# Kernel optimization log

Measured on AMD Instinct MI355X. Metric: run time of the kernel, lower is better.

The kernel has to match this reference:

```python
import jax, jax.numpy as jnp
import numpy as np

D_MODEL = 1024
N_HEADS = 16
D_HEAD = D_MODEL // N_HEADS
HIDDEN = 4096
B, T = 2, 2048
EPS = 1e-5


def setup_inputs() -> dict:
    key = jax.random.key(0)
    ks = jax.random.split(key, 16)
    s = 0.02
    return {
        "x": jax.random.normal(ks[0], (B, T, D_MODEL), dtype=jnp.float32),
        # LayerNorm 1
        "gamma1": jnp.ones((D_MODEL,), jnp.float32),
        "beta1": jnp.zeros((D_MODEL,), jnp.float32),
        # attention projections, stored (in, out) so y = x @ W + b
        "Wq": jax.random.normal(ks[1], (D_MODEL, D_MODEL), jnp.float32) * s,
        "bq": jnp.zeros((D_MODEL,), jnp.float32),
        "Wk": jax.random.normal(ks[2], (D_MODEL, D_MODEL), jnp.float32) * s,
        "bk": jnp.zeros((D_MODEL,), jnp.float32),
        "Wv": jax.random.normal(ks[3], (D_MODEL, D_MODEL), jnp.float32) * s,
        "bv": jnp.zeros((D_MODEL,), jnp.float32),
        "Wo": jax.random.normal(ks[4], (D_MODEL, D_MODEL), jnp.float32) * s,
        "bo": jnp.zeros((D_MODEL,), jnp.float32),
        # LayerNorm 2
        "gamma2": jnp.ones((D_MODEL,), jnp.float32),
        "beta2": jnp.zeros((D_MODEL,), jnp.float32),
        # MLP
        "W1": jax.random.normal(ks[5], (D_MODEL, HIDDEN), jnp.float32) * s,
        "b1": jnp.zeros((HIDDEN,), jnp.float32),
        "W2": jax.random.normal(ks[6], (HIDDEN, D_MODEL), jnp.float32) * s,
        "b2": jnp.zeros((D_MODEL,), jnp.float32),
    }


def _layernorm(x, gamma, beta):
    mean = jnp.mean(x, axis=-1, keepdims=True)
    var = jnp.mean(jnp.square(x - mean), axis=-1, keepdims=True)  # unbiased=False
    return gamma * (x - mean) * jax.lax.rsqrt(var + EPS) + beta


def _attention(x, Wq, bq, Wk, bk, Wv, bv, Wo, bo):
    b, t, _ = x.shape
    q = (x @ Wq + bq).reshape(b, t, N_HEADS, D_HEAD)
    k = (x @ Wk + bk).reshape(b, t, N_HEADS, D_HEAD)
    v = (x @ Wv + bv).reshape(b, t, N_HEADS, D_HEAD)
    scores = jnp.einsum("bqhd,bkhd->bhqk", q, k) / np.sqrt(D_HEAD).astype(np.float32)
    causal = jnp.tril(jnp.ones((t, t), dtype=bool))  # keep j <= i
    scores = jnp.where(causal, scores, -jnp.inf)
    attn = jax.nn.softmax(scores, axis=-1)
    out = jnp.einsum("bhqk,bkhd->bqhd", attn, v).reshape(b, t, D_MODEL)
    return out @ Wo + bo


def reference(x, gamma1, beta1, Wq, bq, Wk, bk, Wv, bv, Wo, bo,
              gamma2, beta2, W1, b1, W2, b2):
    # x = x + Attn(LN1(x))
    x = x + _attention(_layernorm(x, gamma1, beta1), Wq, bq, Wk, bk, Wv, bv, Wo, bo)
    # x = x + MLP(LN2(x)); torch F.gelu default = exact erf gelu
    h = _layernorm(x, gamma2, beta2)
    h = jax.nn.gelu(h @ W1 + b1, approximate=False) @ W2 + b2
    return x + h
```

## Files before the change

### kernel.cpp

```cpp
#include <hip/hip_runtime.h>
#include <stdint.h>

typedef unsigned short u16;
typedef short bf16x8 __attribute__((ext_vector_type(8)));
typedef float f32x4 __attribute__((ext_vector_type(4)));
typedef float f32x16 __attribute__((ext_vector_type(16)));

#define MB (1024L*1024L)

__device__ inline u16 f2bf(float f) {
  union { float f; unsigned u; } v; v.f = f;
  unsigned r = (v.u + 0x7FFFu + ((v.u >> 16) & 1u)) >> 16;
  return (u16)r;
}

__device__ inline float bf2f(u16 u) {
  union { unsigned u; float f; } v; v.u = ((unsigned)u) << 16; return v.f;
}

__device__ inline unsigned cvtpk(float lo, float hi) {
  unsigned r;
  asm("v_cvt_pk_bf16_f32 %0, %1, %2" : "=v"(r) : "v"(lo), "v"(hi));
  return r;
}

#define GLOAD16(gptr, lptr) \
  __builtin_amdgcn_global_load_lds((__attribute__((address_space(1))) void*)(gptr), \
                                   (__attribute__((address_space(3))) void*)(lptr), 16, 0, 0)

__global__ __launch_bounds__(256) void twconv(const float* __restrict__ W,
                                              u16* __restrict__ WT, int K, int N) {
  __shared__ float tile[32][33];
  const int nbn = N >> 5;
  const int bk = blockIdx.x / nbn;
  const int bn = blockIdx.x % nbn;
  const int tid = threadIdx.x;
  const int r = tid >> 3;
  const int c4 = (tid & 7) << 2;
  const float4 v = *(const float4*)(W + (size_t)(bk * 32 + r) * N + bn * 32 + c4);
  tile[r][c4 + 0] = v.x; tile[r][c4 + 1] = v.y;
  tile[r][c4 + 2] = v.z; tile[r][c4 + 3] = v.w;
  __syncthreads();
  ushort4 o;
  o.x = f2bf(tile[c4 + 0][r]); o.y = f2bf(tile[c4 + 1][r]);
  o.z = f2bf(tile[c4 + 2][r]); o.w = f2bf(tile[c4 + 3][r]);
  *(ushort4*)(WT + (size_t)(bn * 32 + r) * K + bk * 32 + c4) = o;
}

__global__ __launch_bounds__(256) void concat3(const float* __restrict__ a,
                                               const float* __restrict__ b,
                                               const float* __restrict__ c,
                                               float* __restrict__ out, int n) {
  int i = blockIdx.x * 256 + threadIdx.x;
  if (i < n) { out[i] = a[i]; out[n + i] = b[i]; out[2 * n + i] = c[i]; }
}

__global__ __launch_bounds__(256) void ln_kernel(const float* __restrict__ x,
                                                 const float* __restrict__ gamma,
                                                 const float* __restrict__ beta,
                                                 u16* __restrict__ out) {
  const int row = blockIdx.x;
  const int tid = threadIdx.x;
  const float4 v = *(const float4*)(x + (size_t)row * 1024 + tid * 4);
  float s = v.x + v.y + v.z + v.w;
  float s2 = v.x * v.x + v.y * v.y + v.z * v.z + v.w * v.w;
#pragma unroll
  for (int m = 1; m < 64; m <<= 1) {
    s += __shfl_xor(s, m, 64);
    s2 += __shfl_xor(s2, m, 64);
  }
  __shared__ float red[8];
  const int w = tid >> 6;
  if ((tid & 63) == 0) { red[w] = s; red[4 + w] = s2; }
  __syncthreads();
  s = red[0] + red[1] + red[2] + red[3];
  s2 = red[4] + red[5] + red[6] + red[7];
  const float mean = s * (1.0f / 1024.0f);
  const float var = s2 * (1.0f / 1024.0f) - mean * mean;
  const float rstd = rsqrtf(var + 1e-5f);
  const float4 g = *(const float4*)(gamma + tid * 4);
  const float4 b = *(const float4*)(beta + tid * 4);
  ushort4 o;
  o.x = f2bf(g.x * (v.x - mean) * rstd + b.x);
  o.y = f2bf(g.y * (v.y - mean) * rstd + b.y);
  o.z = f2bf(g.z * (v.z - mean) * rstd + b.z);
  o.w = f2bf(g.w * (v.w - mean) * rstd + b.w);
  *(ushort4*)(out + (size_t)row * 1024 + tid * 4) = o;
}

template <int EPI, int BN>
__global__ __launch_bounds__(256, (BN == 64) ? 3 : 2)
void gemm_bt(const u16* __restrict__ A, const u16* __restrict__ BT,
             const float* __restrict__ bias, const float* __restrict__ res,
             void* __restrict__ outp, int M, int N, int K) {
  constexpr int MF = (BN == 128) ? 4 : 2;
  constexpr int ACH = 4;
  constexpr int BCH = BN / 32;
  constexpr int LOADS = ACH + BCH;
  __shared__ __align__(16) u16 As[2][128 * 64];
  __shared__ __align__(16) u16 Bs[2][BN * 64];
  const int nBN = N / BN;
  const int hw = blockIdx.x;
  const int xcd = hw & 7;
  const int rr = hw >> 3;
  const int bm = xcd * 4 + rr / nBN;
  const int bn = rr % nBN;
  const int tid = threadIdx.x;
  const int lane = tid & 63;
  const int wid = tid >> 6;
  const int wm = (BN == 128) ? (wid >> 1) : wid;
  const int wn = (BN == 128) ? (wid & 1) : 0;
  const int e4 = lane >> 4;

  int abase[MF], ax[MF];
#pragma unroll
  for (int m = 0; m < MF; ++m) {
    int rowa = wm * (MF * 16) + m * 16 + (lane & 15);
    abase[m] = rowa * 64; ax[m] = rowa & 7;
  }
  int bbase[4], bx[4];
#pragma unroll
  for (int n = 0; n < 4; ++n) {
    int rowb = wn * 64 + n * 16 + (lane & 15);
    bbase[n] = rowb * 64; bx[n] = rowb & 7;
  }

  size_t ga[ACH]; int loa[ACH];
#pragma unroll
  for (int c = 0; c < ACH; ++c) {
    int idx = tid + (c << 8);
    int row = idx >> 3;
    int ch = (idx & 7) ^ (row & 7);
    ga[c] = (size_t)(bm * 128 + row) * K + (ch << 3);
    loa[c] = idx << 4;
  }
  size_t gb[BCH]; int lob[BCH];
#pragma unroll
  for (int c = 0; c < BCH; ++c) {
    int idx = tid + (c << 8);
    int row = idx >> 3;
    int ch = (idx & 7) ^ (row & 7);
    gb[c] = (size_t)(bn * BN + row) * K + (ch << 3);
    lob[c] = idx << 4;
  }

#define STAGE_G(t, bb) do { \
  _Pragma("unroll") for (int c = 0; c < ACH; ++c) \
    GLOAD16(A + ga[c] + (size_t)(t) * 64, (char*)As[bb] + loa[c]); \
  _Pragma("unroll") for (int c = 0; c < BCH; ++c) \
    GLOAD16(BT + gb[c] + (size_t)(t) * 64, (char*)Bs[bb] + lob[c]); \
} while (0)

  f32x4 acc[MF][4] = {};
  const int nt = K >> 6;

  STAGE_G(0, 0);
  STAGE_G(1, 1);

  for (int t = 0; t < nt; ++t) {
    if (t + 1 < nt) {
      asm volatile("s_waitcnt vmcnt(%0)" :: "i"(LOADS) : "memory");
    } else {
      asm volatile("s_waitcnt vmcnt(0)" ::: "memory");
    }
    __builtin_amdgcn_s_barrier();
    const u16* Ap = As[t & 1];
    const u16* Bp = Bs[t & 1];
    bf16x8 af[2][MF], bfr[2][4];
#pragma unroll
    for (int kk = 0; kk < 2; ++kk) {
#pragma unroll
      for (int m = 0; m < MF; ++m)
        af[kk][m] = *(const bf16x8*)(Ap + abase[m] + (((((kk << 2) | e4)) ^ ax[m]) << 3));
#pragma unroll
      for (int n = 0; n < 4; ++n)
        bfr[kk][n] = *(const bf16x8*)(Bp + bbase[n] + (((((kk << 2) | e4)) ^ bx[n]) << 3));
    }
    asm volatile("s_waitcnt lgkmcnt(0)" ::: "memory");
    __builtin_amdgcn_s_barrier();
    if (t + 2 < nt) STAGE_G(t + 2, t & 1);
    __builtin_amdgcn_s_setprio(1);
#pragma unroll
    for (int kk = 0; kk < 2; ++kk)
#pragma unroll
      for (int m = 0; m < MF; ++m)
#pragma unroll
        for (int n = 0; n < 4; ++n)
          acc[m][n] = __builtin_amdgcn_mfma_f32_16x16x32_bf16(af[kk][m], bfr[kk][n], acc[m][n], 0, 0, 0);
    __builtin_amdgcn_s_setprio(0);
  }
#undef STAGE_G

  const int rbase = bm * 128 + wm * (MF * 16);
  const int cbase = bn * BN + wn * 64;
#pragma unroll
  for (int m = 0; m < MF; ++m) {
#pragma unroll
    for (int n = 0; n < 4; ++n) {
      const int col = cbase + n * 16 + (lane & 15);
      const int row0 = rbase + m * 16 + ((lane >> 4) << 2);
      const float bv = bias[col];
#pragma unroll
      for (int r = 0; r < 4; ++r) {
        const int row = row0 + r;
        float v = acc[m][n][r] + bv;
        if (EPI == 1) {
          ((float*)outp)[(size_t)row * N + col] = v + res[(size_t)row * N + col];
        } else if (EPI == 2) {
          float tt = v * (1.0f + 0.044715f * v * v);
          float sg = 1.0f / (1.0f + __expf(-1.5957691216057308f * tt));
          ((u16*)outp)[(size_t)row * N + col] = f2bf(v * sg);
        } else {
          ((u16*)outp)[(size_t)row * N + col] = f2bf(v);
        }
      }
    }
  }
}

__global__ __launch_bounds__(512, 2) void attn_kernel(const u16* __restrict__ QKV,
                                                      u16* __restrict__ O) {
  __shared__ __align__(16) u16 SM[5][4096];
  const int T = 2048, LD = 3072;
  const int blk = blockIdx.x;
  const int xcd = blk & 7;
  const int i = blk >> 3;
  const int bh = xcd * 4 + (i & 3);
  const int p = i >> 2;
  const int b = bh >> 4, hd = bh & 15;
  const int tid = threadIdx.x;
  const int lane = tid & 63;
  const int w = tid >> 6;
  const int h = lane >> 5;
  const int cA = p, cB = 15 - p;
  const int myc = (w < 4) ? cA : cB;
  const int qwb = myc * 128 + (w & 3) * 32;
  const int qg = qwb + (lane & 31);
  const int diag = qwb >> 6;
  const int myNt = diag + 1;
  const int nt = 2 * cB + 2;

  const u16* Qb = QKV + (size_t)b * T * LD + hd * 64;
  const u16* Kb = Qb + 1024;
  const u16* Vb = Qb + 2048;

  const float QSC = 0.18033688011112042f;
  bf16x8 qf[4];
#pragma unroll
  for (int s = 0; s < 4; ++s) {
    bf16x8 raw = *(const bf16x8*)(Qb + (size_t)qg * LD + s * 16 + h * 8);
    union { unsigned wd[4]; bf16x8 v; } u;
#pragma unroll
    for (int e = 0; e < 4; ++e)
      u.wd[e] = cvtpk(bf2f((u16)raw[2 * e]) * QSC, bf2f((u16)raw[2 * e + 1]) * QSC);
    qf[s] = u.v;
  }

  f32x16 oacc[2] = {};
  f32x16 sacc[2];
  union PF { unsigned wd[4]; bf16x8 v; } pf[4];
  float m = -INFINITY, l = 0.0f;

  const int srow = tid >> 3;
  const int scol = tid & 7;
  const int kgc = ((scol ^ (srow & 7)) << 3);

#define VWRITE(buf, vvreg) do { \
  _Pragma("unroll") for (int e = 0; e < 8; ++e) { \
    int d = scol * 8 + e; \
    SM[2 + (buf)][(d << 6) | (srow & 7) | ((((srow >> 3) ^ e ^ scol) & 7) << 3)] = (u16)(vvreg)[e]; \
  } \
} while (0)

  GLOAD16(Kb + (size_t)srow * LD + kgc, (char*)SM[0] + tid * 16);
  {
    bf16x8 vv0 = *(const bf16x8*)(Vb + (size_t)srow * LD + scol * 8);
    VWRITE(0, vv0);
  }
  __syncthreads();

  int vPrev = 2, vCur = 0, vNext = 1;
  for (int j = 0; j < nt; ++j) {
    const bool pre = (j + 1 < nt);
    bf16x8 vv;
    if (pre) {
      GLOAD16(Kb + (size_t)((j + 1) * 64 + srow) * LD + kgc, (char*)SM[(j + 1) & 1] + tid * 16);
      vv = *(const bf16x8*)(Vb + (size_t)((j + 1) * 64 + srow) * LD + scol * 8);
    }
    const bool doQK = (j < myNt);
    const bool doPV = (j >= 1) && (j <= myNt);

    __builtin_amdgcn_s_setprio(1);
    if (doQK) {
      const u16* Kp = SM[j & 1];
#pragma unroll
      for (int t = 0; t < 2; ++t) {
#pragma unroll
        for (int r = 0; r < 16; ++r) sacc[t][r] = 0.0f;
#pragma unroll
        for (int s = 0; s < 4; ++s) {
          int row = t * 32 + (lane & 31);
          bf16x8 kf = *(const bf16x8*)(Kp + (row << 6) + ((((2 * s + h) ^ (row & 7)) & 7) << 3));
          sacc[t] = __builtin_amdgcn_mfma_f32_32x32x16_bf16(kf, qf[s], sacc[t], 0, 0, 0);
        }
      }
    }
    if (doPV) {
      const u16* Vp = SM[2 + vPrev];
#pragma unroll
      for (int d2 = 0; d2 < 2; ++d2) {
        int d = d2 * 32 + (lane & 31);
#pragma unroll
        for (int ks = 0; ks < 4; ++ks) {
          bf16x8 vf = *(const bf16x8*)(Vp + (d << 6) + ((((2 * ks + h) ^ (d & 7) ^ ((d >> 3) & 7)) & 7) << 3));
          oacc[d2] = __builtin_amdgcn_mfma_f32_32x32x16_bf16(vf, pf[ks].v, oacc[d2], 0, 0, 0);
        }
      }
    }
    __builtin_amdgcn_s_setprio(0);

    if (doQK) {
      if (j == diag) {
#pragma unroll
        for (int t = 0; t < 2; ++t)
#pragma unroll
          for (int r = 0; r < 16; ++r) {
            int key = (j << 6) + 32 * t + (r & 3) + 8 * (r >> 2) + 4 * h;
            if (key > qg) sacc[t][r] = -INFINITY;
          }
      }

      float pmax = -INFINITY;
#pragma unroll
      for (int t = 0; t < 2; ++t)
#pragma unroll
        for (int r = 0; r < 16; ++r) pmax = fmaxf(pmax, sacc[t][r]);
      pmax = fmaxf(pmax, __shfl_xor(pmax, 32, 64));

      if (!__all(pmax - m <= 2.8853900817779268f)) {
        float mn = fmaxf(m, pmax);
        float alpha = exp2f(m - mn);
        m = mn;
        l *= alpha;
#pragma unroll
        for (int d2 = 0; d2 < 2; ++d2)
#pragma unroll
          for (int r = 0; r < 16; ++r) oacc[d2][r] *= alpha;
      }

      float lsum = 0.0f;
#pragma unroll
      for (int t = 0; t < 2; ++t)
#pragma unroll
        for (int r = 0; r < 16; ++r) {
          float pe = exp2f(sacc[t][r] - m);
          sacc[t][r] = pe;
          lsum += pe;
        }
      lsum += __shfl_xor(lsum, 32, 64);
      l += lsum;

#pragma unroll
      for (int t = 0; t < 2; ++t) {
#pragma unroll
        for (int kb = 0; kb < 2; ++kb) {
          int base = 8 * kb;
          unsigned A0 = cvtpk(sacc[t][base + 0], sacc[t][base + 1]);
          unsigned A2 = cvtpk(sacc[t][base + 2], sacc[t][base + 3]);
          unsigned A4 = cvtpk(sacc[t][base + 4], sacc[t][base + 5]);
          unsigned A6 = cvtpk(sacc[t][base + 6], sacc[t][base + 7]);
          unsigned S0 = (unsigned)__shfl_xor((int)(h ? A0 : A4), 32, 64);
          unsigned S2 = (unsigned)__shfl_xor((int)(h ? A2 : A6), 32, 64);
          PF& u = pf[2 * t + kb];
          u.wd[0] = h ? S0 : A0;
          u.wd[1] = h ? S2 : A2;
          u.wd[2] = h ? A4 : S0;
          u.wd[3] = h ? A6 : S2;
        }
      }
    }

    if (pre) VWRITE(vNext, vv);
    __syncthreads();
    vPrev = vCur; vCur = vNext; vNext = (vNext == 2) ? 0 : (vNext + 1);
  }

  if (myNt == nt) {
    const u16* Vp = SM[2 + vPrev];
#pragma unroll
    for (int d2 = 0; d2 < 2; ++d2) {
      int d = d2 * 32 + (lane & 31);
#pragma unroll
      for (int ks = 0; ks < 4; ++ks) {
        bf16x8 vf = *(const bf16x8*)(Vp + (d << 6) + ((((2 * ks + h) ^ (d & 7) ^ ((d >> 3) & 7)) & 7) << 3));
        oacc[d2] = __builtin_amdgcn_mfma_f32_32x32x16_bf16(vf, pf[ks].v, oacc[d2], 0, 0, 0);
      }
    }
  }
  __syncthreads();

  const float rinv = 1.0f / l;
  u16* Ob = (u16*)SM;
  const int qloc = w * 32 + (lane & 31);
#pragma unroll
  for (int d2 = 0; d2 < 2; ++d2)
#pragma unroll
    for (int r = 0; r < 16; ++r) {
      int d = d2 * 32 + (r & 3) + 8 * (r >> 2) + 4 * h;
      Ob[(qloc << 6) | (d ^ ((qloc & 7) << 3))] = f2bf(oacc[d2][r] * rinv);
    }
  __syncthreads();
#pragma unroll
  for (int it = 0; it < 4; ++it) {
    int r = (tid >> 3) + it * 64;
    int c = tid & 7;
    bf16x8 val = *(const bf16x8*)(Ob + (r << 6) + (((c ^ (r & 7)) & 7) << 3));
    int qg2 = (r < 128) ? (cA * 128 + r) : (cB * 128 + (r - 128));
    *(bf16x8*)(O + (size_t)(b * T + qg2) * 1024 + hd * 64 + c * 8) = val;
  }
}

extern "C" void kernel_launch(void* const* d_in, const int* in_sizes, int n_in,
                              void* d_out, int out_size, void* d_ws, size_t ws_size,
                              hipStream_t stream) {
  const float* x      = (const float*)d_in[0];
  const float* gamma1 = (const float*)d_in[1];
  const float* beta1  = (const float*)d_in[2];
  const float* Wq     = (const float*)d_in[3];
  const float* bq     = (const float*)d_in[4];
  const float* Wk     = (const float*)d_in[5];
  const float* bk     = (const float*)d_in[6];
  const float* Wv     = (const float*)d_in[7];
  const float* bv     = (const float*)d_in[8];
  const float* Wo     = (const float*)d_in[9];
  const float* bo     = (const float*)d_in[10];
  const float* gamma2 = (const float*)d_in[11];
  const float* beta2  = (const float*)d_in[12];
  const float* W1     = (const float*)d_in[13];
  const float* b1     = (const float*)d_in[14];
  const float* W2     = (const float*)d_in[15];
  const float* b2     = (const float*)d_in[16];

  char* ws = (char*)d_ws;
  u16* WqkvT = (u16*)(ws + 0 * MB);
  u16* WoT   = (u16*)(ws + 6 * MB);
  u16* W1T   = (u16*)(ws + 8 * MB);
  u16* W2T   = (u16*)(ws + 16 * MB);
  u16* qkv   = (u16*)(ws + 24 * MB);
  u16* hb    = (u16*)(ws + 24 * MB);
  u16* xn    = (u16*)(ws + 56 * MB);
  float* bqkv = (float*)d_out;
  float* x1 = (float*)d_out;

  const int M = 4096;

  twconv<<<dim3(1024), dim3(256), 0, stream>>>(Wq, WqkvT, 1024, 1024);
  twconv<<<dim3(1024), dim3(256), 0, stream>>>(Wk, WqkvT + 1024 * 1024, 1024, 1024);
  twconv<<<dim3(1024), dim3(256), 0, stream>>>(Wv, WqkvT + 2048 * 1024, 1024, 1024);
  twconv<<<dim3(1024), dim3(256), 0, stream>>>(Wo, WoT, 1024, 1024);
  twconv<<<dim3(4096), dim3(256), 0, stream>>>(W1, W1T, 1024, 4096);
  twconv<<<dim3(4096), dim3(256), 0, stream>>>(W2, W2T, 4096, 1024);
  concat3<<<dim3(4), dim3(256), 0, stream>>>(bq, bk, bv, bqkv, 1024);

  ln_kernel<<<dim3(M), dim3(256), 0, stream>>>(x, gamma1, beta1, xn);

  gemm_bt<0, 128><<<dim3(768), dim3(256), 0, stream>>>(xn, WqkvT, bqkv, nullptr, qkv, M, 3072, 1024);

  attn_kernel<<<dim3(256), dim3(512), 0, stream>>>(qkv, xn);

  gemm_bt<1, 64><<<dim3(512), dim3(256), 0, stream>>>(xn, WoT, bo, x, x1, M, 1024, 1024);

  ln_kernel<<<dim3(M), dim3(256), 0, stream>>>(x1, gamma2, beta2, xn);

  gemm_bt<2, 128><<<dim3(1024), dim3(256), 0, stream>>>(xn, W1T, b1, nullptr, hb, M, 4096, 1024);
  gemm_bt<1, 64><<<dim3(512), dim3(256), 0, stream>>>(hb, W2T, b2, x1, d_out, M, 1024, 4096);
}
```

Baseline: 239.6 us.

## Fuse weight prep and LN1 into one kernel; split attention KV tiles across warp pairs

Merges the six weight-transpose launches, the bias concat and the first LayerNorm into a single wprep kernel, removing several launch gaps. Attention now uses 64-row query chunks with twice as many blocks. Within each block, warp pairs split the KV tiles by parity (split-K style) and merge their partial softmax state and outputs through LDS at the end. This raises attention parallelism and load balance, at the cost of more LDS (8 buffers), a cross-warp merge step, and processing two KV tiles per sync.

```diff
diff --git a/kernel.cpp b/kernel.cpp
--- a/kernel.cpp
+++ b/kernel.cpp
@@ -28,31 +28,77 @@
   __builtin_amdgcn_global_load_lds((__attribute__((address_space(1))) void*)(gptr), \
                                    (__attribute__((address_space(3))) void*)(lptr), 16, 0, 0)
 
-__global__ __launch_bounds__(256) void twconv(const float* __restrict__ W,
-                                              u16* __restrict__ WT, int K, int N) {
+__global__ __launch_bounds__(256) void wprep(
+    const float* __restrict__ Wq, const float* __restrict__ Wk,
+    const float* __restrict__ Wv, const float* __restrict__ Wo,
+    const float* __restrict__ W1, const float* __restrict__ W2,
+    const float* __restrict__ bq, const float* __restrict__ bk,
+    const float* __restrict__ bv,
+    u16* __restrict__ WqkvT, u16* __restrict__ WoT,
+    u16* __restrict__ W1T, u16* __restrict__ W2T, float* __restrict__ bqkv,
+    const float* __restrict__ x, const float* __restrict__ gamma1,
+    const float* __restrict__ beta1, u16* __restrict__ xn) {
+  const int blk = blockIdx.x;
+  const int tid = threadIdx.x;
   __shared__ float tile[32][33];
+  __shared__ float red[8];
+
+  if (blk >= 12292) {
+    const int row = blk - 12292;
+    const float4 v = *(const float4*)(x + (size_t)row * 1024 + tid * 4);
+    float s = v.x + v.y + v.z + v.w;
+    float s2 = v.x * v.x + v.y * v.y + v.z * v.z + v.w * v.w;
+#pragma unroll
+    for (int mm = 1; mm < 64; mm <<= 1) {
+      s += __shfl_xor(s, mm, 64);
+      s2 += __shfl_xor(s2, mm, 64);
+    }
+    const int w = tid >> 6;
+    if ((tid & 63) == 0) { red[w] = s; red[4 + w] = s2; }
+    __syncthreads();
+    s = red[0] + red[1] + red[2] + red[3];
+    s2 = red[4] + red[5] + red[6] + red[7];
+    const float mean = s * (1.0f / 1024.0f);
+    const float var = s2 * (1.0f / 1024.0f) - mean * mean;
+    const float rstd = rsqrtf(var + 1e-5f);
+    const float4 g = *(const float4*)(gamma1 + tid * 4);
+    const float4 bb = *(const float4*)(beta1 + tid * 4);
+    ushort4 o;
+    o.x = f2bf(g.x * (v.x - mean) * rstd + bb.x);
+    o.y = f2bf(g.y * (v.y - mean) * rstd + bb.y);
+    o.z = f2bf(g.z * (v.z - mean) * rstd + bb.z);
+    o.w = f2bf(g.w * (v.w - mean) * rstd + bb.w);
+    *(ushort4*)(xn + (size_t)row * 1024 + tid * 4) = o;
+    return;
+  }
+  if (blk >= 12288) {
+    int i = (blk - 12288) * 256 + tid;
+    bqkv[i] = bq[i]; bqkv[1024 + i] = bk[i]; bqkv[2048 + i] = bv[i];
+    return;
+  }
+  const float* W; u16* WT; int K, N, tb;
+  if (blk < 4096) {
+    K = 1024; N = 1024;
+    if (blk < 1024)      { W = Wq; WT = WqkvT;               tb = blk; }
+    else if (blk < 2048) { W = Wk; WT = WqkvT + 1024 * 1024; tb = blk - 1024; }
+    else if (blk < 3072) { W = Wv; WT = WqkvT + 2048 * 1024; tb = blk - 2048; }
+    else                 { W = Wo; WT = WoT;                 tb = blk - 3072; }
+  } else if (blk < 8192) { W = W1; WT = W1T; K = 1024; N = 4096; tb = blk - 4096; }
+  else                   { W = W2; WT = W2T; K = 4096; N = 1024; tb = blk - 8192; }
+
   const int nbn = N >> 5;
-  const int bk = blockIdx.x / nbn;
-  const int bn = blockIdx.x % nbn;
-  const int tid = threadIdx.x;
+  const int bk_ = tb / nbn;
+  const int bn = tb % nbn;
   const int r = tid >> 3;
   const int c4 = (tid & 7) << 2;
-  const float4 v = *(const float4*)(W + (size_t)(bk * 32 + r) * N + bn * 32 + c4);
+  const float4 v = *(const float4*)(W + (size_t)(bk_ * 32 + r) * N + bn * 32 + c4);
   tile[r][c4 + 0] = v.x; tile[r][c4 + 1] = v.y;
   tile[r][c4 + 2] = v.z; tile[r][c4 + 3] = v.w;
   __syncthreads();
   ushort4 o;
   o.x = f2bf(tile[c4 + 0][r]); o.y = f2bf(tile[c4 + 1][r]);
   o.z = f2bf(tile[c4 + 2][r]); o.w = f2bf(tile[c4 + 3][r]);
-  *(ushort4*)(WT + (size_t)(bn * 32 + r) * K + bk * 32 + c4) = o;
-}
-
-__global__ __launch_bounds__(256) void concat3(const float* __restrict__ a,
-                                               const float* __restrict__ b,
-                                               const float* __restrict__ c,
-                                               float* __restrict__ out, int n) {
-  int i = blockIdx.x * 256 + threadIdx.x;
-  if (i < n) { out[i] = a[i]; out[n + i] = b[i]; out[2 * n + i] = c[i]; }
+  *(ushort4*)(WT + (size_t)(bn * 32 + r) * K + bk_ * 32 + c4) = o;
 }
 
 __global__ __launch_bounds__(256) void ln_kernel(const float* __restrict__ x,
@@ -220,7 +266,7 @@
 
 __global__ __launch_bounds__(512, 2) void attn_kernel(const u16* __restrict__ QKV,
                                                       u16* __restrict__ O) {
-  __shared__ __align__(16) u16 SM[5][4096];
+  __shared__ __align__(16) u16 SM[8][4096];
   const int T = 2048, LD = 3072;
   const int blk = blockIdx.x;
   const int xcd = blk & 7;
@@ -232,13 +278,15 @@
   const int lane = tid & 63;
   const int w = tid >> 6;
   const int h = lane >> 5;
-  const int cA = p, cB = 15 - p;
-  const int myc = (w < 4) ? cA : cB;
-  const int qwb = myc * 128 + (w & 3) * 32;
-  const int qg = qwb + (lane & 31);
-  const int diag = qwb >> 6;
-  const int myNt = diag + 1;
-  const int nt = 2 * cB + 2;
+  const int grp = w >> 2;
+  const int wr = w & 1;
+  const int par = (w >> 1) & 1;
+  const int cA = p, cB = 31 - p;
+  const int myc = grp ? cB : cA;
+  const int qg = myc * 64 + wr * 32 + (lane & 31);
+  const int myNt = myc + 1;
+  const int nt = cB + 1;
+  const int ni = (nt + 1) >> 1;
 
   const u16* Qb = QKV + (size_t)b * T * LD + hd * 64;
   const u16* Kb = Qb + 1024;
@@ -268,31 +316,38 @@
 #define VWRITE(buf, vvreg) do { \
   _Pragma("unroll") for (int e = 0; e < 8; ++e) { \
     int d = scol * 8 + e; \
-    SM[2 + (buf)][(d << 6) | (srow & 7) | ((((srow >> 3) ^ e ^ scol) & 7) << 3)] = (u16)(vvreg)[e]; \
+    SM[4 + (buf)][(d << 6) | (srow & 7) | ((((srow >> 3) ^ e ^ scol) & 7) << 3)] = (u16)(vvreg)[e]; \
   } \
 } while (0)
 
   GLOAD16(Kb + (size_t)srow * LD + kgc, (char*)SM[0] + tid * 16);
+  GLOAD16(Kb + (size_t)(64 + srow) * LD + kgc, (char*)SM[1] + tid * 16);
   {
-    bf16x8 vv0 = *(const bf16x8*)(Vb + (size_t)srow * LD + scol * 8);
-    VWRITE(0, vv0);
+    bf16x8 va = *(const bf16x8*)(Vb + (size_t)srow * LD + scol * 8);
+    bf16x8 vb = *(const bf16x8*)(Vb + (size_t)(64 + srow) * LD + scol * 8);
+    VWRITE(0, va);
+    VWRITE(1, vb);
   }
   __syncthreads();
 
-  int vPrev = 2, vCur = 0, vNext = 1;
-  for (int j = 0; j < nt; ++j) {
-    const bool pre = (j + 1 < nt);
-    bf16x8 vv;
-    if (pre) {
-      GLOAD16(Kb + (size_t)((j + 1) * 64 + srow) * LD + kgc, (char*)SM[(j + 1) & 1] + tid * 16);
-      vv = *(const bf16x8*)(Vb + (size_t)((j + 1) * 64 + srow) * LD + scol * 8);
-    }
-    const bool doQK = (j < myNt);
-    const bool doPV = (j >= 1) && (j <= myNt);
-
-    __builtin_amdgcn_s_setprio(1);
-    if (doQK) {
-      const u16* Kp = SM[j & 1];
+  for (int it = 0; it < ni; ++it) {
+    const int j0 = 2 * it, j1 = j0 + 1;
+    const bool pre0 = (j0 + 2 < nt);
+    const bool pre1 = (j1 + 2 < nt);
+    bf16x8 vv0, vv1;
+    if (pre0) {
+      GLOAD16(Kb + (size_t)((j0 + 2) * 64 + srow) * LD + kgc, (char*)SM[(j0 + 2) & 3] + tid * 16);
+      vv0 = *(const bf16x8*)(Vb + (size_t)((j0 + 2) * 64 + srow) * LD + scol * 8);
+    }
+    if (pre1) {
+      GLOAD16(Kb + (size_t)((j1 + 2) * 64 + srow) * LD + kgc, (char*)SM[(j1 + 2) & 3] + tid * 16);
+      vv1 = *(const bf16x8*)(Vb + (size_t)((j1 + 2) * 64 + srow) * LD + scol * 8);
+    }
+
+    const int jm = j0 + par;
+    if (jm < myNt) {
+      const u16* Kp = SM[jm & 3];
+      __builtin_amdgcn_s_setprio(1);
 #pragma unroll
       for (int t = 0; t < 2; ++t) {
 #pragma unroll
@@ -304,28 +359,14 @@
           sacc[t] = __builtin_amdgcn_mfma_f32_32x32x16_bf16(kf, qf[s], sacc[t], 0, 0, 0);
         }
       }
-    }
-    if (doPV) {
-      const u16* Vp = SM[2 + vPrev];
-#pragma unroll
-      for (int d2 = 0; d2 < 2; ++d2) {
-        int d = d2 * 32 + (lane & 31);
-#pragma unroll
-        for (int ks = 0; ks < 4; ++ks) {
-          bf16x8 vf = *(const bf16x8*)(Vp + (d << 6) + ((((2 * ks + h) ^ (d & 7) ^ ((d >> 3) & 7)) & 7) << 3));
-          oacc[d2] = __builtin_amdgcn_mfma_f32_32x32x16_bf16(vf, pf[ks].v, oacc[d2], 0, 0, 0);
-        }
-      }
-    }
-    __builtin_amdgcn_s_setprio(0);
-
-    if (doQK) {
-      if (j == diag) {
+      __builtin_amdgcn_s_setprio(0);
+
+      if (jm == myc) {
 #pragma unroll
         for (int t = 0; t < 2; ++t)
 #pragma unroll
           for (int r = 0; r < 16; ++r) {
-            int key = (j << 6) + 32 * t + (r & 3) + 8 * (r >> 2) + 4 * h;
+            int key = (jm << 6) + 32 * t + (r & 3) + 8 * (r >> 2) + 4 * h;
             if (key > qg) sacc[t][r] = -INFINITY;
           }
       }
@@ -378,44 +419,66 @@
           u.wd[3] = h ? A6 : S2;
         }
       }
-    }
-
-    if (pre) VWRITE(vNext, vv);
+
+      const u16* Vp = SM[4 + (jm & 3)];
+      __builtin_amdgcn_s_setprio(1);
+#pragma unroll
+      for (int d2 = 0; d2 < 2; ++d2) {
+        int d = d2 * 32 + (lane & 31);
+#pragma unroll
+        for (int ks = 0; ks < 4; ++ks) {
+          bf16x8 vf = *(const bf16x8*)(Vp + (d << 6) + ((((2 * ks + h) ^ (d & 7) ^ ((d >> 3) & 7)) & 7) << 3));
+          oacc[d2] = __builtin_amdgcn_mfma_f32_32x32x16_bf16(vf, pf[ks].v, oacc[d2], 0, 0, 0);
+        }
+      }
+      __builtin_amdgcn_s_setprio(0);
+    }
+
+    if (pre0) VWRITE((j0 + 2) & 3, vv0);
+    if (pre1) VWRITE((j1 + 2) & 3, vv1);
     __syncthreads();
-    vPrev = vCur; vCur = vNext; vNext = (vNext == 2) ? 0 : (vNext + 1);
-  }
-
-  if (myNt == nt) {
-    const u16* Vp = SM[2 + vPrev];
-#pragma unroll
-    for (int d2 = 0; d2 < 2; ++d2) {
-      int d = d2 * 32 + (lane & 31);
-#pragma unroll
-      for (int ks = 0; ks < 4; ++ks) {
-        bf16x8 vf = *(const bf16x8*)(Vp + (d << 6) + ((((2 * ks + h) ^ (d & 7) ^ ((d >> 3) & 7)) & 7) << 3));
-        oacc[d2] = __builtin_amdgcn_mfma_f32_32x32x16_bf16(vf, pf[ks].v, oacc[d2], 0, 0, 0);
-      }
-    }
+  }
+#undef VWRITE
+
+  float* dumpO = (float*)SM;
+  float* dumpML = (float*)((char*)SM + 32768);
+  u16* Ob = (u16*)((char*)SM + 40960);
+  const int slot = grp * 2 + wr;
+  if (par == 1) {
+    float* dO = dumpO + (slot * 64 + lane) * 32;
+#pragma unroll
+    for (int d2 = 0; d2 < 2; ++d2)
+#pragma unroll
+      for (int r = 0; r < 16; ++r) dO[d2 * 16 + r] = oacc[d2][r];
+    dumpML[(slot * 64 + lane) * 2 + 0] = m;
+    dumpML[(slot * 64 + lane) * 2 + 1] = l;
   }
   __syncthreads();
-
-  const float rinv = 1.0f / l;
-  u16* Ob = (u16*)SM;
-  const int qloc = w * 32 + (lane & 31);
-#pragma unroll
-  for (int d2 = 0; d2 < 2; ++d2)
-#pragma unroll
-    for (int r = 0; r < 16; ++r) {
-      int d = d2 * 32 + (r & 3) + 8 * (r >> 2) + 4 * h;
-      Ob[(qloc << 6) | (d ^ ((qloc & 7) << 3))] = f2bf(oacc[d2][r] * rinv);
-    }
+  if (par == 0) {
+    const float* dO = dumpO + (slot * 64 + lane) * 32;
+    float m1 = dumpML[(slot * 64 + lane) * 2 + 0];
+    float l1 = dumpML[(slot * 64 + lane) * 2 + 1];
+    float mM = fmaxf(m, m1);
+    float a0 = exp2f(m - mM), a1 = exp2f(m1 - mM);
+    float lm = l * a0 + l1 * a1;
+    float rinv = 1.0f / lm;
+    const int row = slot * 32 + (lane & 31);
+#pragma unroll
+    for (int d2 = 0; d2 < 2; ++d2)
+#pragma unroll
+      for (int r = 0; r < 16; ++r) {
+        float ov = (oacc[d2][r] * a0 + dO[d2 * 16 + r] * a1) * rinv;
+        int d = d2 * 32 + (r & 3) + 8 * (r >> 2) + 4 * h;
+        Ob[(row << 6) | (d ^ ((row & 7) << 3))] = f2bf(ov);
+      }
+  }
   __syncthreads();
 #pragma unroll
-  for (int it = 0; it < 4; ++it) {
-    int r = (tid >> 3) + it * 64;
+  for (int it2 = 0; it2 < 2; ++it2) {
+    int r = (tid >> 3) + it2 * 64;
     int c = tid & 7;
     bf16x8 val = *(const bf16x8*)(Ob + (r << 6) + (((c ^ (r & 7)) & 7) << 3));
-    int qg2 = (r < 128) ? (cA * 128 + r) : (cB * 128 + (r - 128));
+    int qg2 = ((r < 64) ? cA : cB) * 64 + (r & 63);
     *(bf16x8*)(O + (size_t)(b * T + qg2) * 1024 + hd * 64 + c * 8) = val;
   }
 }
@@ -454,19 +517,13 @@
 
   const int M = 4096;
 
-  twconv<<<dim3(1024), dim3(256), 0, stream>>>(Wq, WqkvT, 1024, 1024);
-  twconv<<<dim3(1024), dim3(256), 0, stream>>>(Wk, WqkvT + 1024 * 1024, 1024, 1024);
-  twconv<<<dim3(1024), dim3(256), 0, stream>>>(Wv, WqkvT + 2048 * 1024, 1024, 1024);
-  twconv<<<dim3(1024), dim3(256), 0, stream>>>(Wo, WoT, 1024, 1024);
-  twconv<<<dim3(4096), dim3(256), 0, stream>>>(W1, W1T, 1024, 4096);
-  twconv<<<dim3(4096), dim3(256), 0, stream>>>(W2, W2T, 4096, 1024);
-  concat3<<<dim3(4), dim3(256), 0, stream>>>(bq, bk, bv, bqkv, 1024);
-
-  ln_kernel<<<dim3(M), dim3(256), 0, stream>>>(x, gamma1, beta1, xn);
+  wprep<<<dim3(16388), dim3(256), 0, stream>>>(Wq, Wk, Wv, Wo, W1, W2, bq, bk, bv,
+                                               WqkvT, WoT, W1T, W2T, bqkv,
+                                               x, gamma1, beta1, xn);
 
   gemm_bt<0, 128><<<dim3(768), dim3(256), 0, stream>>>(xn, WqkvT, bqkv, nullptr, qkv, M, 3072, 1024);
 
-  attn_kernel<<<dim3(256), dim3(512), 0, stream>>>(qkv, xn);
+  attn_kernel<<<dim3(512), dim3(512), 0, stream>>>(qkv, xn);
 
   gemm_bt<1, 64><<<dim3(512), dim3(256), 0, stream>>>(xn, WoT, bo, x, x1, M, 1024, 1024);
 
```

Result: faster. 226.2 us (-5.6%).
